# Optimization experiments

Measured on AMD Instinct MI355X. Metric: run time of the kernel, lower is better.

The kernel has to match this reference:

```python
import jax, jax.numpy as jnp
import numpy as np

BATCH, SEQ_LEN, VOCAB, DIM = 64, 512, 32000, 512


def setup_inputs() -> dict:
    key = jax.random.key(0)
    k = jax.random.split(key, 6)
    s = 1.0 / np.sqrt(DIM)
    return {
        "x": jax.random.randint(k[0], (BATCH, SEQ_LEN), 0, VOCAB),
        "emb": jax.random.normal(k[1], (VOCAB, DIM), dtype=jnp.float32),
        "W_ih": jax.random.normal(k[2], (DIM, DIM), dtype=jnp.float32) * s,
        "W_hh": jax.random.normal(k[3], (DIM, DIM), dtype=jnp.float32) * s,
        "b_ih": jax.random.normal(k[4], (DIM,), dtype=jnp.float32) * s,
        "b_hh": jax.random.normal(k[5], (DIM,), dtype=jnp.float32) * s,
    }


def reference(x, emb, W_ih, W_hh, b_ih, b_hh):
    # Embedding lookup: [B, T, I]
    xe = emb[x]
    # Precompute input projections for all timesteps: [T, B, H]
    xp = jnp.einsum("bti,hi->tbh", xe, W_ih) + b_ih + b_hh
    h0 = jnp.zeros((x.shape[0], W_hh.shape[0]), dtype=xe.dtype)

    def step(h, xp_t):
        h_new = jnp.tanh(xp_t + h @ W_hh.T)
        return h_new, h_new

    _, hiddens = jax.lax.scan(step, h0, xp)  # [T, B, H]
    hiddens = jnp.transpose(hiddens, (1, 2, 0))  # [B, H, T]
    return jax.nn.softmax(hiddens, axis=1)
```

## Files before the change

kernel.cpp:

```cpp
#include <hip/hip_runtime.h>
#include <cstdint>

#define BATCH 64
#define SEQ   512
#define DIM   512
#define MTOT  (BATCH*SEQ)

#define CSL 8
#define GRP 32
#define RPG 2

__global__ __launch_bounds__(128) void pack_w(const float* __restrict__ W,
                                              float4* __restrict__ Wpk,
                                              unsigned long long* __restrict__ hpair) {
    const int c  = blockIdx.x;
    const int jb = threadIdx.x;
    const float4 v = *(const float4*)&W[(size_t)c * DIM + 4 * jb];
    Wpk[(size_t)jb * DIM + c] = v;
    hpair[(size_t)blockIdx.x * 128 + threadIdx.x] = 0ull;
}

__global__ __launch_bounds__(256) void embed_proj(
    const int*   __restrict__ xidx,
    const float* __restrict__ emb,
    const float* __restrict__ W_ih,
    const float* __restrict__ b_ih,
    const float* __restrict__ b_hh,
    float*       __restrict__ xp) {
    __shared__ float As[64][68];
    __shared__ float Bs[64][68];

    const int m0  = blockIdx.x * 64;
    const int n0  = blockIdx.y * 64;
    const int tid = threadIdx.x;

    const int lr = tid >> 4;
    const int lc = (tid & 15) << 2;

    int rows[4];
#pragma unroll
    for (int i = 0; i < 4; i++) rows[i] = xidx[m0 + lr + 16 * i];

    const int tm = (tid & 15) << 2;
    const int tn = (tid >> 4) << 2;

    float acc[4][4];
#pragma unroll
    for (int i = 0; i < 4; i++)
#pragma unroll
        for (int j = 0; j < 4; j++) acc[i][j] = 0.0f;

    for (int k0 = 0; k0 < DIM; k0 += 64) {
#pragma unroll
        for (int i = 0; i < 4; i++) {
            const int rl = lr + 16 * i;
            const float4 a = *(const float4*)&emb[(size_t)rows[i] * DIM + k0 + lc];
            As[lc + 0][rl] = a.x; As[lc + 1][rl] = a.y;
            As[lc + 2][rl] = a.z; As[lc + 3][rl] = a.w;
            const float4 b = *(const float4*)&W_ih[(size_t)(n0 + rl) * DIM + k0 + lc];
            Bs[lc + 0][rl] = b.x; Bs[lc + 1][rl] = b.y;
            Bs[lc + 2][rl] = b.z; Bs[lc + 3][rl] = b.w;
        }
        __syncthreads();
#pragma unroll 8
        for (int kk = 0; kk < 64; kk++) {
            const float4 a = *(const float4*)&As[kk][tm];
            const float4 b = *(const float4*)&Bs[kk][tn];
            acc[0][0] = fmaf(a.x, b.x, acc[0][0]);
            acc[0][1] = fmaf(a.x, b.y, acc[0][1]);
            acc[0][2] = fmaf(a.x, b.z, acc[0][2]);
            acc[0][3] = fmaf(a.x, b.w, acc[0][3]);
            acc[1][0] = fmaf(a.y, b.x, acc[1][0]);
            acc[1][1] = fmaf(a.y, b.y, acc[1][1]);
            acc[1][2] = fmaf(a.y, b.z, acc[1][2]);
            acc[1][3] = fmaf(a.y, b.w, acc[1][3]);
            acc[2][0] = fmaf(a.z, b.x, acc[2][0]);
            acc[2][1] = fmaf(a.z, b.y, acc[2][1]);
            acc[2][2] = fmaf(a.z, b.z, acc[2][2]);
            acc[2][3] = fmaf(a.z, b.w, acc[2][3]);
            acc[3][0] = fmaf(a.w, b.x, acc[3][0]);
            acc[3][1] = fmaf(a.w, b.y, acc[3][1]);
            acc[3][2] = fmaf(a.w, b.z, acc[3][2]);
            acc[3][3] = fmaf(a.w, b.w, acc[3][3]);
        }
        __syncthreads();
    }

    const int n = n0 + tn;
    const float bias0 = b_ih[n + 0] + b_hh[n + 0];
    const float bias1 = b_ih[n + 1] + b_hh[n + 1];
    const float bias2 = b_ih[n + 2] + b_hh[n + 2];
    const float bias3 = b_ih[n + 3] + b_hh[n + 3];
#pragma unroll
    for (int i = 0; i < 4; i++) {
        float4 o;
        o.x = acc[i][0] + bias0;
        o.y = acc[i][1] + bias1;
        o.z = acc[i][2] + bias2;
        o.w = acc[i][3] + bias3;
        *(float4*)&xp[(size_t)(m0 + tm + i) * DIM + n] = o;
    }
}

__global__ __launch_bounds__(512, 1)
void rnn_scan(const float4* __restrict__ Wpk, float* __restrict__ buf,
              unsigned long long* __restrict__ hpair) {
    __shared__ float hlds[RPG * DIM];
    __shared__ float part[2 * 8 * RPG * 64];

    const int tid   = threadIdx.x;
    const int slice = blockIdx.x / GRP;
    const int grp   = blockIdx.x % GRP;
    const int c     = tid & 63;
    const int ks    = tid >> 6;
    const int b0    = grp * RPG;
    const int col0  = slice * 64;
    const int hb    = ks * 16;

    float4 wreg[16];
#pragma unroll
    for (int i = 0; i < 16; i++)
        wreg[i] = Wpk[(size_t)(hb + i) * DIM + col0 + c];

    hlds[tid]       = 0.0f;
    hlds[DIM + tid] = 0.0f;

    const int rr = tid >> 6;
    const int cc = tid & 63;
    float xq = 0.0f;
    if (tid < 128)
        xq = buf[((size_t)(b0 + rr) * SEQ + 0) * DIM + col0 + cc];

    for (int t = 0; t < SEQ; t++) {
        if (t > 0) {
            unsigned long long* base =
                hpair + ((size_t)(t & 1) * GRP + grp) * (RPG * DIM);
            unsigned long long v0 = __hip_atomic_load(base + tid,
                                    __ATOMIC_RELAXED, __HIP_MEMORY_SCOPE_AGENT);
            unsigned long long v1 = __hip_atomic_load(base + DIM + tid,
                                    __ATOMIC_RELAXED, __HIP_MEMORY_SCOPE_AGENT);
            const unsigned tgt = (unsigned)t;
            while (((unsigned)(v0 >> 32) != tgt) | ((unsigned)(v1 >> 32) != tgt)) {
                __builtin_amdgcn_s_sleep(1);
                v0 = __hip_atomic_load(base + tid,
                                    __ATOMIC_RELAXED, __HIP_MEMORY_SCOPE_AGENT);
                v1 = __hip_atomic_load(base + DIM + tid,
                                    __ATOMIC_RELAXED, __HIP_MEMORY_SCOPE_AGENT);
            }
            hlds[tid]       = __uint_as_float((unsigned)v0);
            hlds[DIM + tid] = __uint_as_float((unsigned)v1);
        }

        float p0 = 0.f, p1 = 0.f;
        const float4* h4 = (const float4*)hlds;
#pragma unroll
        for (int i = 0; i < 16; i++) {
            const float4 w  = wreg[i];
            const float4 h0 = h4[0 * 128 + hb + i];
            const float4 h1 = h4[1 * 128 + hb + i];
            p0 = fmaf(w.x, h0.x, p0); p0 = fmaf(w.y, h0.y, p0);
            p0 = fmaf(w.z, h0.z, p0); p0 = fmaf(w.w, h0.w, p0);
            p1 = fmaf(w.x, h1.x, p1); p1 = fmaf(w.y, h1.y, p1);
            p1 = fmaf(w.z, h1.z, p1); p1 = fmaf(w.w, h1.w, p1);
        }
        const int pb = (t & 1) << 10;
        part[pb + ks * 128 +  0 + c] = p0;
        part[pb + ks * 128 + 64 + c] = p1;
        __syncthreads();

        if (tid < 128) {
            float s = part[pb + tid];
#pragma unroll
            for (int k = 1; k < 8; k++) s += part[pb + k * 128 + tid];
            const float hn = tanhf(xq + s);
            if (t + 1 < SEQ) {
                const unsigned long long pv =
                    ((unsigned long long)(unsigned)(t + 1) << 32) |
                    (unsigned long long)__float_as_uint(hn);
                __hip_atomic_store(
                    hpair + (((size_t)((t + 1) & 1) * GRP + grp) * RPG + rr) * DIM
                          + col0 + cc,
                    pv, __ATOMIC_RELAXED, __HIP_MEMORY_SCOPE_AGENT);
            }
            buf[((size_t)(b0 + rr) * SEQ + t) * DIM + col0 + cc] = hn;
            const int tn = (t + 1 < SEQ) ? (t + 1) : t;
            xq = buf[((size_t)(b0 + rr) * SEQ + tn) * DIM + col0 + cc];
        }
    }
}

__global__ __launch_bounds__(256) void softmax_T(const float* __restrict__ hid,
                                                 float* __restrict__ out) {
    __shared__ float rowmax[64];
    __shared__ float rowinv[64];
    __shared__ float tile[64][65];

    const int b   = blockIdx.x;
    const int t0  = blockIdx.y * 64;
    const int tid = threadIdx.x;
    const float* base = hid + ((size_t)b * SEQ + t0) * DIM;

    const int r = tid >> 2;
    const int p = tid & 3;

    float m = -1e30f;
#pragma unroll 4
    for (int k = 0; k < 32; k++) {
        const float4 v = *(const float4*)&base[r * DIM + ((k * 4 + p) << 2)];
        m = fmaxf(m, fmaxf(fmaxf(v.x, v.y), fmaxf(v.z, v.w)));
    }
    m = fmaxf(m, __shfl_xor(m, 1));
    m = fmaxf(m, __shfl_xor(m, 2));

    float s = 0.0f;
#pragma unroll 4
    for (int k = 0; k < 32; k++) {
        const float4 v = *(const float4*)&base[r * DIM + ((k * 4 + p) << 2)];
        s += expf(v.x - m) + expf(v.y - m) + expf(v.z - m) + expf(v.w - m);
    }
    s += __shfl_xor(s, 1);
    s += __shfl_xor(s, 2);
    if (p == 0) {
        rowmax[r] = m;
        rowinv[r] = 1.0f / s;
    }
    __syncthreads();

    for (int hc = 0; hc < 8; hc++) {
#pragma unroll
        for (int i = 0; i < 16; i++) {
            const int lin = tid + 256 * i;
            const int rr  = lin >> 6;
            const int ccc = lin & 63;
            const float v = base[rr * DIM + hc * 64 + ccc];
            tile[ccc][rr] = expf(v - rowmax[rr]) * rowinv[rr];
        }
        __syncthreads();
#pragma unroll
        for (int i = 0; i < 16; i++) {
            const int lin = tid + 256 * i;
            const int hh  = lin >> 6;
            const int tt  = lin & 63;
            out[((size_t)b * DIM + hc * 64 + hh) * SEQ + t0 + tt] = tile[hh][tt];
        }
        __syncthreads();
    }
}

extern "C" void kernel_launch(void* const* d_in, const int* in_sizes, int n_in,
                              void* d_out, int out_size, void* d_ws, size_t ws_size,
                              hipStream_t stream) {
    const int*   x    = (const int*)  d_in[0];
    const float* emb  = (const float*)d_in[1];
    const float* W_ih = (const float*)d_in[2];
    const float* W_hh = (const float*)d_in[3];
    const float* b_ih = (const float*)d_in[4];
    const float* b_hh = (const float*)d_in[5];
    float* out = (float*)d_out;

    float* buf = (float*)d_ws;
    float4* Wpk = (float4*)out;
    unsigned long long* hpair =
        (unsigned long long*)(out + (4 << 20));

    pack_w<<<dim3(DIM), 128, 0, stream>>>(W_hh, Wpk, hpair);
    embed_proj<<<dim3(MTOT / 64, DIM / 64), 256, 0, stream>>>(x, emb, W_ih, b_ih, b_hh, buf);
    rnn_scan<<<CSL * GRP, 512, 0, stream>>>(Wpk, buf, hpair);
    softmax_T<<<dim3(BATCH, SEQ / 64), 256, 0, stream>>>(buf, out);
}
```

Before: 1.234 ms.

## Broadcast hidden state via readlane instead of LDS in RNN scan

Each wave already polls exactly the 64 hidden values its K-slice needs. The new code keeps them in registers and broadcasts them with readlane, which removes the LDS staging of h on every timestep. It also splits each dot product into two accumulators for more ILP, packs the partial sums as float2 for the cross-wave reduction, and pins the weight registers with empty asm. Launch bounds are raised to allow 2 blocks per CU, and addressing is precomputed. The aim is lower per-step latency on the serial recurrence, at the cost of many scalar readlane instructions and possible register-pressure changes.

After: 1.288 ms. 1.04x slower.

```diff
diff --git a/kernel.cpp b/kernel.cpp
--- a/kernel.cpp
+++ b/kernel.cpp
@@ -9,6 +9,7 @@
 #define CSL 8
 #define GRP 32
 #define RPG 2
+#define SLOT (GRP*RPG*DIM)
 
 __global__ __launch_bounds__(128) void pack_w(const float* __restrict__ W,
                                               float4* __restrict__ Wpk,
@@ -102,11 +103,10 @@
     }
 }
 
-__global__ __launch_bounds__(512, 1)
+__global__ __launch_bounds__(512, 2)
 void rnn_scan(const float4* __restrict__ Wpk, float* __restrict__ buf,
               unsigned long long* __restrict__ hpair) {
-    __shared__ float hlds[RPG * DIM];
-    __shared__ float part[2 * 8 * RPG * 64];
+    __shared__ float2 part2[2][8][64];
 
     const int tid   = threadIdx.x;
     const int slice = blockIdx.x / GRP;
@@ -121,70 +121,88 @@
 #pragma unroll
     for (int i = 0; i < 16; i++)
         wreg[i] = Wpk[(size_t)(hb + i) * DIM + col0 + c];
-
-    hlds[tid]       = 0.0f;
-    hlds[DIM + tid] = 0.0f;
+#pragma unroll
+    for (int i = 0; i < 16; i++)
+        asm volatile("" : "+v"(wreg[i].x), "+v"(wreg[i].y),
+                          "+v"(wreg[i].z), "+v"(wreg[i].w));
+
+    unsigned long long* const pollb = hpair + (size_t)grp * (RPG * DIM) + tid;
 
     const int rr = tid >> 6;
     const int cc = tid & 63;
     float xq = 0.0f;
-    if (tid < 128)
-        xq = buf[((size_t)(b0 + rr) * SEQ + 0) * DIM + col0 + cc];
+    size_t bufoff = 0;
+    unsigned long long* pubp = nullptr;
+    if (tid < 128) {
+        bufoff = (size_t)(b0 + rr) * SEQ * DIM + col0 + cc;
+        xq     = buf[bufoff];
+        pubp   = hpair + ((size_t)grp * RPG + rr) * DIM + col0 + cc;
+    }
+
+    unsigned h0u = 0, h1u = 0;
 
     for (int t = 0; t < SEQ; t++) {
         if (t > 0) {
-            unsigned long long* base =
-                hpair + ((size_t)(t & 1) * GRP + grp) * (RPG * DIM);
-            unsigned long long v0 = __hip_atomic_load(base + tid,
-                                    __ATOMIC_RELAXED, __HIP_MEMORY_SCOPE_AGENT);
-            unsigned long long v1 = __hip_atomic_load(base + DIM + tid,
-                                    __ATOMIC_RELAXED, __HIP_MEMORY_SCOPE_AGENT);
+            unsigned long long* bp = pollb + (size_t)(t & 1) * SLOT;
+            unsigned long long v0 = __hip_atomic_load(bp,       __ATOMIC_RELAXED,
+                                                      __HIP_MEMORY_SCOPE_AGENT);
+            unsigned long long v1 = __hip_atomic_load(bp + DIM, __ATOMIC_RELAXED,
+                                                      __HIP_MEMORY_SCOPE_AGENT);
             const unsigned tgt = (unsigned)t;
             while (((unsigned)(v0 >> 32) != tgt) | ((unsigned)(v1 >> 32) != tgt)) {
                 __builtin_amdgcn_s_sleep(1);
-                v0 = __hip_atomic_load(base + tid,
-                                    __ATOMIC_RELAXED, __HIP_MEMORY_SCOPE_AGENT);
-                v1 = __hip_atomic_load(base + DIM + tid,
-                                    __ATOMIC_RELAXED, __HIP_MEMORY_SCOPE_AGENT);
+                v0 = __hip_atomic_load(bp,       __ATOMIC_RELAXED,
+                                       __HIP_MEMORY_SCOPE_AGENT);
+                v1 = __hip_atomic_load(bp + DIM, __ATOMIC_RELAXED,
+                                       __HIP_MEMORY_SCOPE_AGENT);
             }
-            hlds[tid]       = __uint_as_float((unsigned)v0);
-            hlds[DIM + tid] = __uint_as_float((unsigned)v1);
-        }
-
-        float p0 = 0.f, p1 = 0.f;
-        const float4* h4 = (const float4*)hlds;
+            h0u = (unsigned)v0;
+            h1u = (unsigned)v1;
+        }
+
+        float p0a = 0.f, p0b = 0.f, p1a = 0.f, p1b = 0.f;
 #pragma unroll
         for (int i = 0; i < 16; i++) {
-            const float4 w  = wreg[i];
-            const float4 h0 = h4[0 * 128 + hb + i];
-            const float4 h1 = h4[1 * 128 + hb + i];
-            p0 = fmaf(w.x, h0.x, p0); p0 = fmaf(w.y, h0.y, p0);
-            p0 = fmaf(w.z, h0.z, p0); p0 = fmaf(w.w, h0.w, p0);
-            p1 = fmaf(w.x, h1.x, p1); p1 = fmaf(w.y, h1.y, p1);
-            p1 = fmaf(w.z, h1.z, p1); p1 = fmaf(w.w, h1.w, p1);
-        }
-        const int pb = (t & 1) << 10;
-        part[pb + ks * 128 +  0 + c] = p0;
-        part[pb + ks * 128 + 64 + c] = p1;
+            const float4 w = wreg[i];
+            const float a0 = __uint_as_float(__builtin_amdgcn_readlane(h0u, 4*i+0));
+            const float a1 = __uint_as_float(__builtin_amdgcn_readlane(h0u, 4*i+1));
+            const float a2 = __uint_as_float(__builtin_amdgcn_readlane(h0u, 4*i+2));
+            const float a3 = __uint_as_float(__builtin_amdgcn_readlane(h0u, 4*i+3));
+            p0a = fmaf(w.x, a0, p0a); p0b = fmaf(w.y, a1, p0b);
+            p0a = fmaf(w.z, a2, p0a); p0b = fmaf(w.w, a3, p0b);
+            const float b0v = __uint_as_float(__builtin_amdgcn_readlane(h1u, 4*i+0));
+            const float b1v = __uint_as_float(__builtin_amdgcn_readlane(h1u, 4*i+1));
+            const float b2v = __uint_as_float(__builtin_amdgcn_readlane(h1u, 4*i+2));
+            const float b3v = __uint_as_float(__builtin_amdgcn_readlane(h1u, 4*i+3));
+            p1a = fmaf(w.x, b0v, p1a); p1b = fmaf(w.y, b1v, p1b);
+            p1a = fmaf(w.z, b2v, p1a); p1b = fmaf(w.w, b3v, p1b);
+        }
+
+        part2[t & 1][ks][c] = make_float2(p0a + p0b, p1a + p1b);
         __syncthreads();
 
         if (tid < 128) {
-            float s = part[pb + tid];
-#pragma unroll
-            for (int k = 1; k < 8; k++) s += part[pb + k * 128 + tid];
+            const float* pp = (const float*)&part2[t & 1][0][0];
+            const int bix = cc * 2 + rr;
+            float s = pp[bix];
+            s += pp[bix + 128];
+            s += pp[bix + 256];
+            s += pp[bix + 384];
+            s += pp[bix + 512];
+            s += pp[bix + 640];
+            s += pp[bix + 768];
+            s += pp[bix + 896];
             const float hn = tanhf(xq + s);
             if (t + 1 < SEQ) {
                 const unsigned long long pv =
                     ((unsigned long long)(unsigned)(t + 1) << 32) |
                     (unsigned long long)__float_as_uint(hn);
-                __hip_atomic_store(
-                    hpair + (((size_t)((t + 1) & 1) * GRP + grp) * RPG + rr) * DIM
-                          + col0 + cc,
-                    pv, __ATOMIC_RELAXED, __HIP_MEMORY_SCOPE_AGENT);
+                __hip_atomic_store(pubp + (size_t)((t + 1) & 1) * SLOT, pv,
+                                   __ATOMIC_RELAXED, __HIP_MEMORY_SCOPE_AGENT);
             }
-            buf[((size_t)(b0 + rr) * SEQ + t) * DIM + col0 + cc] = hn;
+            buf[bufoff + (size_t)t * DIM] = hn;
             const int tn = (t + 1 < SEQ) ? (t + 1) : t;
-            xq = buf[((size_t)(b0 + rr) * SEQ + tn) * DIM + col0 + cc];
+            xq = buf[bufoff + (size_t)tn * DIM];
         }
     }
 }
@@ -230,10 +248,10 @@
 #pragma unroll
         for (int i = 0; i < 16; i++) {
             const int lin = tid + 256 * i;
-            const int rr  = lin >> 6;
+            const int rrr = lin >> 6;
             const int ccc = lin & 63;
-            const float v = base[rr * DIM + hc * 64 + ccc];
-            tile[ccc][rr] = expf(v - rowmax[rr]) * rowinv[rr];
+            const float v = base[rrr * DIM + hc * 64 + ccc];
+            tile[ccc][rrr] = expf(v - rowmax[rrr]) * rowinv[rrr];
         }
         __syncthreads();
 #pragma unroll
```
